# Kernel optimization log

Measured on AMD Instinct MI355X. Metric: run time of the kernel, lower is better.

## Reference

```python
import jax, jax.numpy as jnp
import numpy as np

N = 32768
LATENT = 2
HID = 100
STEPS = 100

swish = jax.nn.swish


def setup_inputs() -> dict:
    key = jax.random.key(0)
    ks = jax.random.split(key, 12)

    def w(k, shape):
        fan_in = shape[0]
        return (jax.random.normal(k, shape) / np.sqrt(fan_in)).astype(jnp.float32)

    return {
        "x": jax.random.normal(ks[0], (N, 3), dtype=jnp.float32),
        # encoder: 3 -> 100 -> 100 -> (mu: 2, log_t: 1)
        "We1": w(ks[1], (3, HID)), "be1": jnp.zeros((HID,), jnp.float32),
        "We2": w(ks[2], (HID, HID)), "be2": jnp.zeros((HID,), jnp.float32),
        "Wmu": w(ks[3], (HID, LATENT)), "bmu": jnp.zeros((LATENT,), jnp.float32),
        "Wlt": w(ks[4], (HID, 1)), "blt": jnp.zeros((1,), jnp.float32),
        # decoder: 2 -> 100 -> (mu: 3, log_sigma: 3)
        "Wd1": w(ks[5], (LATENT, HID)), "bd1": jnp.zeros((HID,), jnp.float32),
        "Wdmu": w(ks[6], (HID, 3)), "bdmu": jnp.zeros((3,), jnp.float32),
        "Wds": w(ks[7], (HID, 3)), "bds": jnp.zeros((3,), jnp.float32),
        # prior layer biases
        "b_muz": jnp.zeros((LATENT,), jnp.float32),
        "b_ltz": jnp.zeros((1,), jnp.float32),
        # standard-normal noise for the 100-step SDE (dW = sqrt(dt) * noise)
        "noise": jax.random.normal(ks[8], (STEPS, N, LATENT), dtype=jnp.float32),
    }


def reference(x, We1, be1, We2, be2, Wmu, bmu, Wlt, blt,
              Wd1, bd1, Wdmu, bdmu, Wds, bds, b_muz, b_ltz, noise):
    x = x.astype(jnp.float32)

    # ---- decoder heads on a single latent point z: (LATENT,) ----
    def dec_mu(z):
        return swish(z @ Wd1 + bd1) @ Wdmu + bdmu      # (3,)

    def dec_ls(z):
        return swish(z @ Wd1 + bd1) @ Wds + bds        # (3,)

    def G(z):  # pullback metric, (LATENT, LATENT)
        Jmu = jax.jacfwd(dec_mu)(z)   # (3, LATENT)
        Jsg = jax.jacfwd(dec_ls)(z)   # (3, LATENT)
        return Jmu.T @ Jmu + Jsg.T @ Jsg

    def step_one(z, dW):  # one Euler-Maruyama step for one point
        g = G(z)
        ginv = jnp.linalg.inv(g)
        Dg = jax.jacfwd(G)(z)         # (LATENT, LATENT, LATENT): dG[k,m]/dz_l
        Chris = 0.5 * (jnp.einsum('im,kml->ikl', ginv, Dg)
                       + jnp.einsum('im,lmk->ikl', ginv, Dg)
                       - jnp.einsum('im,klm->ikl', ginv, Dg))
        det = 0.5 * jnp.einsum('jk,ijk->i', ginv, Chris)
        stoch = ginv @ dW
        return (z + det + stoch).astype(jnp.float32)

    # ---- encoder ----
    h = swish(x @ We1 + be1)
    h = swish(h @ We2 + be2)
    mu_zx = h @ Wmu + bmu            # (N, LATENT)
    log_t_zx = h @ Wlt + blt         # (N, 1)

    # ---- Riemannian Brownian-motion sampling (Local) ----
    t = jnp.exp(2.0 * log_t_zx)[:, 0]        # (N,)
    dt = t / STEPS                            # (N,), constant over steps
    dW = jnp.sqrt(dt)[None, :, None] * noise  # (STEPS, N, LATENT)

    def scan_step(z, dW_t):
        return jax.vmap(step_one)(z, dW_t), None

    z, _ = jax.lax.scan(scan_step, mu_zx, dW)

    # ---- prior + decoder outputs ----
    mu_z = b_muz * jnp.ones_like(z)
    log_t_z = b_ltz * jnp.ones((z.shape[0], 1), z.dtype)
    hz = swish(z @ Wd1 + bd1)
    mu_xz = hz @ Wdmu + bdmu
    log_sigma_xz = hz @ Wds + bds

    return (z, mu_xz, log_sigma_xz, mu_zx, log_t_zx, mu_z, log_t_z)
```

## Files before the change

### kernel.cpp

```cpp
#include <hip/hip_runtime.h>

#define N_PTS 32768
#define HID   100
#define STEPS 100

#define OFF_Z     0
#define OFF_MUXZ  65536
#define OFF_LSXZ  163840
#define OFF_MUZX  262144
#define OFF_LTZX  327680
#define OFF_MUZ   360448
#define OFF_LTZ   425984

typedef float v2f __attribute__((ext_vector_type(2)));

#if __has_builtin(__builtin_elementwise_fma)
#define FMA2(a, b, c) __builtin_elementwise_fma((a), (b), (c))
#else
#define FMA2(a, b, c) ((a) * (b) + (c))
#endif

__device__ __forceinline__ v2f splat(float x) { v2f r; r.x = x; r.y = x; return r; }

__device__ __forceinline__ float qreduce(float v) {
  v += __int_as_float(__builtin_amdgcn_update_dpp(0, __float_as_int(v), 0xB1, 0xF, 0xF, true));
  v += __int_as_float(__builtin_amdgcn_update_dpp(0, __float_as_int(v), 0x4E, 0xF, 0xF, true));
  return v;
}
__device__ __forceinline__ v2f qreduce2(v2f v) {
  v2f r; r.x = qreduce(v.x); r.y = qreduce(v.y); return r;
}

__global__ __launch_bounds__(128, 1) void enc_kernel(
    const float* __restrict__ x,
    const float* __restrict__ We1, const float* __restrict__ be1,
    const float* __restrict__ We2, const float* __restrict__ be2,
    const float* __restrict__ Wmu, const float* __restrict__ bmu,
    const float* __restrict__ Wlt, const float* __restrict__ blt,
    const float* __restrict__ b_muz, const float* __restrict__ b_ltz,
    float* __restrict__ out)
{
  const int tid = threadIdx.x;
  const int w   = tid >> 6;
  const int pb  = tid & 63;
  const int p   = blockIdx.x * 64 + pb;
  const int ob  = __builtin_amdgcn_readfirstlane(w * 50);

  const float x0 = x[p*3+0], x1 = x[p*3+1], x2 = x[p*3+2];

  v2f acc2[25];
  #pragma unroll
  for (int i = 0; i < 25; ++i) { acc2[i].x = 0.f; acc2[i].y = 0.f; }

  for (int k = 0; k < HID; ++k) {
    float a   = fmaf(x0, We1[k], fmaf(x1, We1[HID+k], fmaf(x2, We1[2*HID+k], be1[k])));
    float sig = 1.f / (1.f + __expf(-a));
    float h1  = a * sig;
    const v2f hh = splat(h1);
    const v2f* row2 = (const v2f*)(We2 + k*HID + ob);
    #pragma unroll
    for (int oo = 0; oo < 25; ++oo) acc2[oo] = FMA2(hh, row2[oo], acc2[oo]);
  }

  float m0 = 0.f, m1 = 0.f, lt = 0.f;
  #pragma unroll
  for (int oo = 0; oo < 25; ++oo) {
    #pragma unroll
    for (int h = 0; h < 2; ++h) {
      const int o = ob + 2*oo + h;
      float a   = (h ? acc2[oo].y : acc2[oo].x) + be2[o];
      float sig = 1.f / (1.f + __expf(-a));
      float h2  = a * sig;
      m0 = fmaf(h2, Wmu[o*2+0], m0);
      m1 = fmaf(h2, Wmu[o*2+1], m1);
      lt = fmaf(h2, Wlt[o],     lt);
    }
  }

  __shared__ float red[2][64][3];
  red[w][pb][0] = m0; red[w][pb][1] = m1; red[w][pb][2] = lt;
  __syncthreads();
  if (w == 0) {
    m0 += red[1][pb][0] + bmu[0];
    m1 += red[1][pb][1] + bmu[1];
    lt += red[1][pb][2] + blt[0];
    out[OFF_MUZX + p*2+0] = m0;
    out[OFF_MUZX + p*2+1] = m1;
    out[OFF_LTZX + p]     = lt;
    out[OFF_MUZ  + p*2+0] = b_muz[0];
    out[OFF_MUZ  + p*2+1] = b_muz[1];
    out[OFF_LTZ  + p]     = b_ltz[0];
  }
}

__global__ __launch_bounds__(256, 2) void sde_kernel(
    const float* __restrict__ Wd1,  const float* __restrict__ bd1,
    const float* __restrict__ Wdmu, const float* __restrict__ bdmu,
    const float* __restrict__ Wds,  const float* __restrict__ bds,
    const float* __restrict__ noise,
    float* __restrict__ out)
{
  __shared__ __align__(16) float wrec[HID*12];
  const int tid = threadIdx.x;
  for (int idx = tid; idx < HID*12; idx += 256) {
    const int j = idx / 12, f = idx - j*12;
    const float w0 = Wd1[j], w1 = Wd1[HID + j];
    float v;
    switch (f) {
      case 0:  v = w0; break;
      case 1:  v = w1; break;
      case 2:  v = bd1[j]; break;
      case 3:  v = w0*w0; break;
      case 4:  v = w0*w1; break;
      case 5:  v = w1*w1; break;
      case 6:  v = Wdmu[j*3+0]; break;
      case 7:  v = Wds [j*3+0]; break;
      case 8:  v = Wdmu[j*3+1]; break;
      case 9:  v = Wds [j*3+1]; break;
      case 10: v = Wdmu[j*3+2]; break;
      default: v = Wds [j*3+2]; break;
    }
    wrec[idx] = v;
  }
  __syncthreads();

  const int l     = tid & 3;
  const int p     = blockIdx.x * 64 + (tid >> 2);
  const int jbase = l * 25;

  float z0 = out[OFF_MUZX + p*2+0];
  float z1 = out[OFF_MUZX + p*2+1];
  const float sdt = __expf(out[OFF_LTZX + p]) * 0.1f;

  const float2* __restrict__ noise2 = (const float2*)noise;

  for (int step = 0; step < STEPS; ++step) {
    const float2 nz = noise2[(size_t)step*N_PTS + p];

    v2f Jm2[3], Js2[3], Km01[3], Ks01[3], K2[3];
    #pragma unroll
    for (int o = 0; o < 3; ++o) {
      Jm2[o]=splat(0.f); Js2[o]=splat(0.f);
      Km01[o]=splat(0.f); Ks01[o]=splat(0.f); K2[o]=splat(0.f);
    }

    #pragma unroll 5
    for (int jj = 0; jj < 25; ++jj) {
      const float* r = &wrec[(jbase + jj)*12];
      const float4 wa = *(const float4*)(r);
      const float4 wb = *(const float4*)(r + 4);
      const float4 wc = *(const float4*)(r + 8);
      float a   = fmaf(z0, wa.x, fmaf(z1, wa.y, wa.z));
      float e   = __expf(-a);
      float sig = __builtin_amdgcn_rcpf(1.f + e);
      float t1  = 1.f - sig;
      float pp  = sig * t1;
      float u   = fmaf(a, pp, sig);
      float u2  = pp * fmaf(a, fmaf(-2.f, sig, 1.f), 2.f);
      v2f w01;   w01.x = wa.x;  w01.y = wa.y;
      v2f w0011; w0011.x = wa.w; w0011.y = wb.x;
      v2f c01   = splat(u)  * w01;
      v2f q0001 = splat(u2) * w0011;
      v2f q11s  = splat(u2 * wb.y);
      v2f ws[3];
      ws[0].x = wb.z; ws[0].y = wb.w;
      ws[1].x = wc.x; ws[1].y = wc.y;
      ws[2].x = wc.z; ws[2].y = wc.w;
      #pragma unroll
      for (int o = 0; o < 3; ++o) {
        const v2f mo = splat(ws[o].x);
        const v2f so = splat(ws[o].y);
        Jm2[o]  = FMA2(mo, c01,   Jm2[o]);
        Js2[o]  = FMA2(so, c01,   Js2[o]);
        Km01[o] = FMA2(mo, q0001, Km01[o]);
        Ks01[o] = FMA2(so, q0001, Ks01[o]);
        K2[o]   = FMA2(ws[o], q11s, K2[o]);
      }
    }

    float Jm[3][2], Js[3][2], Km[3][3], Ks[3][3];
    #pragma unroll
    for (int o = 0; o < 3; ++o) {
      v2f t;
      t = qreduce2(Jm2[o]);  Jm[o][0]=t.x; Jm[o][1]=t.y;
      t = qreduce2(Js2[o]);  Js[o][0]=t.x; Js[o][1]=t.y;
      t = qreduce2(Km01[o]); Km[o][0]=t.x; Km[o][1]=t.y;
      t = qreduce2(Ks01[o]); Ks[o][0]=t.x; Ks[o][1]=t.y;
      t = qreduce2(K2[o]);   Km[o][2]=t.x; Ks[o][2]=t.y;
    }

    float G00=0.f, G01=0.f, G11=0.f;
    #pragma unroll
    for (int o = 0; o < 3; ++o) {
      G00 += Jm[o][0]*Jm[o][0] + Js[o][0]*Js[o][0];
      G01 += Jm[o][0]*Jm[o][1] + Js[o][0]*Js[o][1];
      G11 += Jm[o][1]*Jm[o][1] + Js[o][1]*Js[o][1];
    }
    float D00=0.f, D01=0.f, D10=0.f, D11=0.f, D20=0.f, D21=0.f;
    #pragma unroll
    for (int o = 0; o < 3; ++o) {
      D00 += 2.f*(Km[o][0]*Jm[o][0] + Ks[o][0]*Js[o][0]);
      D01 += 2.f*(Km[o][1]*Jm[o][0] + Ks[o][1]*Js[o][0]);
      D10 += Km[o][0]*Jm[o][1] + Jm[o][0]*Km[o][1] + Ks[o][0]*Js[o][1] + Js[o][0]*Ks[o][1];
      D11 += Km[o][1]*Jm[o][1] + Jm[o][0]*Km[o][2] + Ks[o][1]*Js[o][1] + Js[o][0]*Ks[o][2];
      D20 += 2.f*(Km[o][1]*Jm[o][1] + Ks[o][1]*Js[o][1]);
      D21 += 2.f*(Km[o][2]*Jm[o][1] + Ks[o][2]*Js[o][1]);
    }
    const float det = fmaf(G00, G11, -G01*G01);
    const float id  = __builtin_amdgcn_rcpf(det);
    const float i00 = G11*id, i01 = -G01*id, i11 = G00*id;
    const float T000 = D00;
    const float T001 = 2.f*D10 - D01;
    const float T010 = D01;
    const float T011 = D20;
    const float T110 = 2.f*D11 - D20;
    const float T111 = D21;
    const float C00 = 0.5f*(i00*T000 + i01*T001);
    const float C01 = 0.5f*(i00*T010 + i01*T011);
    const float C02 = 0.5f*(i00*T110 + i01*T111);
    const float C10 = 0.5f*(i01*T000 + i11*T001);
    const float C11 = 0.5f*(i01*T010 + i11*T011);
    const float C12 = 0.5f*(i01*T110 + i11*T111);
    const float dr0 = 0.5f*(i00*C00 + 2.f*i01*C01 + i11*C02);
    const float dr1 = 0.5f*(i00*C10 + 2.f*i01*C11 + i11*C12);

    const float dw0 = sdt*nz.x, dw1 = sdt*nz.y;
    z0 += dr0 + i00*dw0 + i01*dw1;
    z1 += dr1 + i01*dw0 + i11*dw1;
  }

  v2f MS[3]; MS[0]=splat(0.f); MS[1]=splat(0.f); MS[2]=splat(0.f);
  #pragma unroll 5
  for (int jj = 0; jj < 25; ++jj) {
    const float* r = &wrec[(jbase + jj)*12];
    const float4 wa = *(const float4*)(r);
    const float4 wb = *(const float4*)(r + 4);
    const float4 wc = *(const float4*)(r + 8);
    float a   = fmaf(z0, wa.x, fmaf(z1, wa.y, wa.z));
    float sig = __builtin_amdgcn_rcpf(1.f + __expf(-a));
    float h   = a * sig;
    const v2f hh = splat(h);
    v2f ws0; ws0.x = wb.z; ws0.y = wb.w;
    v2f ws1; ws1.x = wc.x; ws1.y = wc.y;
    v2f ws2; ws2.x = wc.z; ws2.y = wc.w;
    MS[0] = FMA2(hh, ws0, MS[0]);
    MS[1] = FMA2(hh, ws1, MS[1]);
    MS[2] = FMA2(hh, ws2, MS[2]);
  }
  #pragma unroll
  for (int o = 0; o < 3; ++o) MS[o] = qreduce2(MS[o]);

  if (l == 0) {
    out[OFF_Z + p*2+0] = z0;
    out[OFF_Z + p*2+1] = z1;
    #pragma unroll
    for (int o = 0; o < 3; ++o) {
      out[OFF_MUXZ + p*3 + o] = MS[o].x + bdmu[o];
      out[OFF_LSXZ + p*3 + o] = MS[o].y + bds[o];
    }
  }
}

extern "C" void kernel_launch(void* const* d_in, const int* in_sizes, int n_in,
                              void* d_out, int out_size, void* d_ws, size_t ws_size,
                              hipStream_t stream) {
  (void)in_sizes; (void)n_in; (void)d_ws; (void)ws_size; (void)out_size;
  const float* x    = (const float*)d_in[0];
  const float* We1  = (const float*)d_in[1];
  const float* be1  = (const float*)d_in[2];
  const float* We2  = (const float*)d_in[3];
  const float* be2  = (const float*)d_in[4];
  const float* Wmu  = (const float*)d_in[5];
  const float* bmu  = (const float*)d_in[6];
  const float* Wlt  = (const float*)d_in[7];
  const float* blt  = (const float*)d_in[8];
  const float* Wd1  = (const float*)d_in[9];
  const float* bd1  = (const float*)d_in[10];
  const float* Wdmu = (const float*)d_in[11];
  const float* bdmu = (const float*)d_in[12];
  const float* Wds  = (const float*)d_in[13];
  const float* bds  = (const float*)d_in[14];
  const float* bmz  = (const float*)d_in[15];
  const float* blz  = (const float*)d_in[16];
  const float* noise= (const float*)d_in[17];
  float* out = (float*)d_out;

  enc_kernel<<<512, 128, 0, stream>>>(x, We1, be1, We2, be2, Wmu, bmu, Wlt, blt,
                                      bmz, blz, out);
  sde_kernel<<<512, 256, 0, stream>>>(Wd1, bd1, Wdmu, bdmu, Wds, bds, noise, out);
}
```

Before: 619.0 us.

## Pair hidden units in SDE packed math and split encoder across four waves

The SDE kernel's shared-memory weight table is reorganised so each record holds two hidden units interleaved. The inner loop then computes activations and Jacobian and Hessian accumulations for both units with packed v2f FMAs, and folds them with a horizontal add before the quad reduction. The aim is fewer scalar ops per hidden unit and more use of dual-issue packed FP32, at the cost of more accumulator registers and padding HID to 104. The encoder moves to 256 threads with four waves, each handling a quarter of the output columns, to raise parallelism and cut per-thread register pressure.

```diff
diff --git a/kernel.cpp b/kernel.cpp
--- a/kernel.cpp
+++ b/kernel.cpp
@@ -3,6 +3,8 @@
 #define N_PTS 32768
 #define HID   100
 #define STEPS 100
+#define NPAIR 52
+#define LPP   13
 
 #define OFF_Z     0
 #define OFF_MUXZ  65536
@@ -13,12 +15,15 @@
 #define OFF_LTZ   425984
 
 typedef float v2f __attribute__((ext_vector_type(2)));
+typedef float v4f __attribute__((ext_vector_type(4)));
 
 #if __has_builtin(__builtin_elementwise_fma)
 #define FMA2(a, b, c) __builtin_elementwise_fma((a), (b), (c))
 #else
 #define FMA2(a, b, c) ((a) * (b) + (c))
 #endif
+#define LOv(q) __builtin_shufflevector((q), (q), 0, 1)
+#define HIv(q) __builtin_shufflevector((q), (q), 2, 3)
 
 __device__ __forceinline__ v2f splat(float x) { v2f r; r.x = x; r.y = x; return r; }
 
@@ -27,11 +32,57 @@
   v += __int_as_float(__builtin_amdgcn_update_dpp(0, __float_as_int(v), 0x4E, 0xF, 0xF, true));
   return v;
 }
-__device__ __forceinline__ v2f qreduce2(v2f v) {
-  v2f r; r.x = qreduce(v.x); r.y = qreduce(v.y); return r;
-}
-
-__global__ __launch_bounds__(128, 1) void enc_kernel(
+__device__ __forceinline__ float hqreduce(v2f v) { return qreduce(v.x + v.y); }
+
+template<int NP>
+__device__ __forceinline__ void enc_chunk(
+    int ob, float x0, float x1, float x2,
+    const float* __restrict__ We1, const float* __restrict__ be1,
+    const float* __restrict__ We2, const float* __restrict__ be2,
+    const float* __restrict__ Wmu, const float* __restrict__ Wlt,
+    float& m0, float& m1, float& lt)
+{
+  v2f acc2[NP];
+  #pragma unroll
+  for (int i = 0; i < NP; ++i) acc2[i] = splat(0.f);
+
+  #pragma unroll 2
+  for (int k = 0; k < HID; k += 2) {
+    const v2f w0 = *(const v2f*)(We1 + k);
+    const v2f w1 = *(const v2f*)(We1 + HID + k);
+    const v2f w2 = *(const v2f*)(We1 + 2*HID + k);
+    const v2f bb = *(const v2f*)(be1 + k);
+    v2f aP = FMA2(splat(x0), w0, FMA2(splat(x1), w1, FMA2(splat(x2), w2, bb)));
+    const float e0 = __expf(-aP.x), e1 = __expf(-aP.y);
+    const float s0 = 1.f / (1.f + e0), s1 = 1.f / (1.f + e1);
+    const v2f hh0 = splat(aP.x * s0);
+    const v2f hh1 = splat(aP.y * s1);
+    const v2f* r0 = (const v2f*)(We2 + k*HID + ob);
+    const v2f* r1 = (const v2f*)(We2 + (k+1)*HID + ob);
+    #pragma unroll
+    for (int oo = 0; oo < NP; ++oo) {
+      v2f tacc = FMA2(hh0, r0[oo], acc2[oo]);
+      acc2[oo] = FMA2(hh1, r1[oo], tacc);
+    }
+  }
+
+  m0 = 0.f; m1 = 0.f; lt = 0.f;
+  #pragma unroll
+  for (int oo = 0; oo < NP; ++oo) {
+    #pragma unroll
+    for (int h = 0; h < 2; ++h) {
+      const int o = ob + 2*oo + h;
+      float a   = (h ? acc2[oo].y : acc2[oo].x) + be2[o];
+      float sig = 1.f / (1.f + __expf(-a));
+      float h2  = a * sig;
+      m0 = fmaf(h2, Wmu[o*2+0], m0);
+      m1 = fmaf(h2, Wmu[o*2+1], m1);
+      lt = fmaf(h2, Wlt[o],     lt);
+    }
+  }
+}
+
+__global__ __launch_bounds__(256, 2) void enc_kernel(
     const float* __restrict__ x,
     const float* __restrict__ We1, const float* __restrict__ be1,
     const float* __restrict__ We2, const float* __restrict__ be2,
@@ -44,46 +95,20 @@
   const int w   = tid >> 6;
   const int pb  = tid & 63;
   const int p   = blockIdx.x * 64 + pb;
-  const int ob  = __builtin_amdgcn_readfirstlane(w * 50);
 
   const float x0 = x[p*3+0], x1 = x[p*3+1], x2 = x[p*3+2];
 
-  v2f acc2[25];
-  #pragma unroll
-  for (int i = 0; i < 25; ++i) { acc2[i].x = 0.f; acc2[i].y = 0.f; }
-
-  for (int k = 0; k < HID; ++k) {
-    float a   = fmaf(x0, We1[k], fmaf(x1, We1[HID+k], fmaf(x2, We1[2*HID+k], be1[k])));
-    float sig = 1.f / (1.f + __expf(-a));
-    float h1  = a * sig;
-    const v2f hh = splat(h1);
-    const v2f* row2 = (const v2f*)(We2 + k*HID + ob);
-    #pragma unroll
-    for (int oo = 0; oo < 25; ++oo) acc2[oo] = FMA2(hh, row2[oo], acc2[oo]);
-  }
-
-  float m0 = 0.f, m1 = 0.f, lt = 0.f;
-  #pragma unroll
-  for (int oo = 0; oo < 25; ++oo) {
-    #pragma unroll
-    for (int h = 0; h < 2; ++h) {
-      const int o = ob + 2*oo + h;
-      float a   = (h ? acc2[oo].y : acc2[oo].x) + be2[o];
-      float sig = 1.f / (1.f + __expf(-a));
-      float h2  = a * sig;
-      m0 = fmaf(h2, Wmu[o*2+0], m0);
-      m1 = fmaf(h2, Wmu[o*2+1], m1);
-      lt = fmaf(h2, Wlt[o],     lt);
-    }
-  }
-
-  __shared__ float red[2][64][3];
+  float m0, m1, lt;
+  if (w < 2) enc_chunk<13>(w * 26,            x0, x1, x2, We1, be1, We2, be2, Wmu, Wlt, m0, m1, lt);
+  else       enc_chunk<12>(52 + (w - 2) * 24, x0, x1, x2, We1, be1, We2, be2, Wmu, Wlt, m0, m1, lt);
+
+  __shared__ float red[4][64][3];
   red[w][pb][0] = m0; red[w][pb][1] = m1; red[w][pb][2] = lt;
   __syncthreads();
   if (w == 0) {
-    m0 += red[1][pb][0] + bmu[0];
-    m1 += red[1][pb][1] + bmu[1];
-    lt += red[1][pb][2] + blt[0];
+    m0 += red[1][pb][0] + red[2][pb][0] + red[3][pb][0] + bmu[0];
+    m1 += red[1][pb][1] + red[2][pb][1] + red[3][pb][1] + bmu[1];
+    lt += red[1][pb][2] + red[2][pb][2] + red[3][pb][2] + blt[0];
     out[OFF_MUZX + p*2+0] = m0;
     out[OFF_MUZX + p*2+1] = m1;
     out[OFF_LTZX + p]     = lt;
@@ -100,25 +125,29 @@
     const float* __restrict__ noise,
     float* __restrict__ out)
 {
-  __shared__ __align__(16) float wrec[HID*12];
+  __shared__ __align__(16) float wrec[NPAIR * 24];
   const int tid = threadIdx.x;
-  for (int idx = tid; idx < HID*12; idx += 256) {
-    const int j = idx / 12, f = idx - j*12;
-    const float w0 = Wd1[j], w1 = Wd1[HID + j];
-    float v;
-    switch (f) {
-      case 0:  v = w0; break;
-      case 1:  v = w1; break;
-      case 2:  v = bd1[j]; break;
-      case 3:  v = w0*w0; break;
-      case 4:  v = w0*w1; break;
-      case 5:  v = w1*w1; break;
-      case 6:  v = Wdmu[j*3+0]; break;
-      case 7:  v = Wds [j*3+0]; break;
-      case 8:  v = Wdmu[j*3+1]; break;
-      case 9:  v = Wds [j*3+1]; break;
-      case 10: v = Wdmu[j*3+2]; break;
-      default: v = Wds [j*3+2]; break;
+  for (int idx = tid; idx < NPAIR * 24; idx += 256) {
+    const int pr = idx / 24, f = idx - pr * 24;
+    const int j  = pr * 2 + (f & 1);
+    const int g  = f >> 1;
+    float v = 0.f;
+    if (j < HID) {
+      const float w0 = Wd1[j], w1 = Wd1[HID + j];
+      switch (g) {
+        case 0:  v = w0; break;
+        case 1:  v = w1; break;
+        case 2:  v = bd1[j]; break;
+        case 3:  v = w1 * w1; break;
+        case 4:  v = w0 * w0; break;
+        case 5:  v = w0 * w1; break;
+        case 6:  v = Wdmu[j*3+0]; break;
+        case 7:  v = Wds [j*3+0]; break;
+        case 8:  v = Wdmu[j*3+1]; break;
+        case 9:  v = Wds [j*3+1]; break;
+        case 10: v = Wdmu[j*3+2]; break;
+        default: v = Wds [j*3+2]; break;
+      }
     }
     wrec[idx] = v;
   }
@@ -126,7 +155,8 @@
 
   const int l     = tid & 3;
   const int p     = blockIdx.x * 64 + (tid >> 2);
-  const int jbase = l * 25;
+  const int pbase = l * LPP;
+  const v4f* __restrict__ Rq = (const v4f*)wrec;
 
   float z0 = out[OFF_MUZX + p*2+0];
   float z1 = out[OFF_MUZX + p*2+1];
@@ -135,76 +165,82 @@
   const float2* __restrict__ noise2 = (const float2*)noise;
 
   for (int step = 0; step < STEPS; ++step) {
-    const float2 nz = noise2[(size_t)step*N_PTS + p];
-
-    v2f Jm2[3], Js2[3], Km01[3], Ks01[3], K2[3];
-    #pragma unroll
-    for (int o = 0; o < 3; ++o) {
-      Jm2[o]=splat(0.f); Js2[o]=splat(0.f);
-      Km01[o]=splat(0.f); Ks01[o]=splat(0.f); K2[o]=splat(0.f);
-    }
-
-    #pragma unroll 5
-    for (int jj = 0; jj < 25; ++jj) {
-      const float* r = &wrec[(jbase + jj)*12];
-      const float4 wa = *(const float4*)(r);
-      const float4 wb = *(const float4*)(r + 4);
-      const float4 wc = *(const float4*)(r + 8);
-      float a   = fmaf(z0, wa.x, fmaf(z1, wa.y, wa.z));
-      float e   = __expf(-a);
-      float sig = __builtin_amdgcn_rcpf(1.f + e);
-      float t1  = 1.f - sig;
-      float pp  = sig * t1;
-      float u   = fmaf(a, pp, sig);
-      float u2  = pp * fmaf(a, fmaf(-2.f, sig, 1.f), 2.f);
-      v2f w01;   w01.x = wa.x;  w01.y = wa.y;
-      v2f w0011; w0011.x = wa.w; w0011.y = wb.x;
-      v2f c01   = splat(u)  * w01;
-      v2f q0001 = splat(u2) * w0011;
-      v2f q11s  = splat(u2 * wb.y);
-      v2f ws[3];
-      ws[0].x = wb.z; ws[0].y = wb.w;
-      ws[1].x = wc.x; ws[1].y = wc.y;
-      ws[2].x = wc.z; ws[2].y = wc.w;
+    const float2 nz = noise2[(size_t)step * N_PTS + p];
+
+    v2f Jm[3][2], Js[3][2], Km[3][3], Ks[3][3];
+    #pragma unroll
+    for (int o = 0; o < 3; ++o) {
+      Jm[o][0]=splat(0.f); Jm[o][1]=splat(0.f);
+      Js[o][0]=splat(0.f); Js[o][1]=splat(0.f);
+      Km[o][0]=splat(0.f); Km[o][1]=splat(0.f); Km[o][2]=splat(0.f);
+      Ks[o][0]=splat(0.f); Ks[o][1]=splat(0.f); Ks[o][2]=splat(0.f);
+    }
+    const v2f z0P = splat(z0), z1P = splat(z1);
+
+    #pragma unroll
+    for (int t = 0; t < LPP; ++t) {
+      const v4f* R = Rq + (pbase + t) * 6;
+      const v4f A  = R[0];
+      const v4f B  = R[1];
+      const v4f Cq = R[2];
+      const v4f M0 = R[3], M1 = R[4], M2 = R[5];
+      const v2f W0P  = LOv(A),  W1P  = HIv(A);
+      const v2f bP   = LOv(B),  W11P = HIv(B);
+      const v2f W00P = LOv(Cq), W01P = HIv(Cq);
+
+      v2f aP = FMA2(z0P, W0P, FMA2(z1P, W1P, bP));
+      v2f eP;   eP.x   = __expf(-aP.x);               eP.y   = __expf(-aP.y);
+      v2f dP = splat(1.f) + eP;
+      v2f sigP; sigP.x = __builtin_amdgcn_rcpf(dP.x); sigP.y = __builtin_amdgcn_rcpf(dP.y);
+      const v2f t1P = splat(1.f) - sigP;
+      const v2f ppP = sigP * t1P;
+      const v2f uP  = FMA2(aP, ppP, sigP);
+      const v2f u2P = ppP * FMA2(aP, FMA2(splat(-2.f), sigP, splat(1.f)), splat(2.f));
+      const v2f c0  = uP  * W0P,  c1  = uP  * W1P;
+      const v2f q00 = u2P * W00P, q01 = u2P * W01P, q11 = u2P * W11P;
+
+      const v2f mP[3] = {LOv(M0), LOv(M1), LOv(M2)};
+      const v2f sP[3] = {HIv(M0), HIv(M1), HIv(M2)};
       #pragma unroll
       for (int o = 0; o < 3; ++o) {
-        const v2f mo = splat(ws[o].x);
-        const v2f so = splat(ws[o].y);
-        Jm2[o]  = FMA2(mo, c01,   Jm2[o]);
-        Js2[o]  = FMA2(so, c01,   Js2[o]);
-        Km01[o] = FMA2(mo, q0001, Km01[o]);
-        Ks01[o] = FMA2(so, q0001, Ks01[o]);
-        K2[o]   = FMA2(ws[o], q11s, K2[o]);
+        Jm[o][0] = FMA2(c0,  mP[o], Jm[o][0]);
+        Jm[o][1] = FMA2(c1,  mP[o], Jm[o][1]);
+        Js[o][0] = FMA2(c0,  sP[o], Js[o][0]);
+        Js[o][1] = FMA2(c1,  sP[o], Js[o][1]);
+        Km[o][0] = FMA2(q00, mP[o], Km[o][0]);
+        Km[o][1] = FMA2(q01, mP[o], Km[o][1]);
+        Km[o][2] = FMA2(q11, mP[o], Km[o][2]);
+        Ks[o][0] = FMA2(q00, sP[o], Ks[o][0]);
+        Ks[o][1] = FMA2(q01, sP[o], Ks[o][1]);
+        Ks[o][2] = FMA2(q11, sP[o], Ks[o][2]);
       }
     }
 
-    float Jm[3][2], Js[3][2], Km[3][3], Ks[3][3];
-    #pragma unroll
-    for (int o = 0; o < 3; ++o) {
-      v2f t;
-      t = qreduce2(Jm2[o]);  Jm[o][0]=t.x; Jm[o][1]=t.y;
-      t = qreduce2(Js2[o]);  Js[o][0]=t.x; Js[o][1]=t.y;
-      t = qreduce2(Km01[o]); Km[o][0]=t.x; Km[o][1]=t.y;
-      t = qreduce2(Ks01[o]); Ks[o][0]=t.x; Ks[o][1]=t.y;
-      t = qreduce2(K2[o]);   Km[o][2]=t.x; Ks[o][2]=t.y;
+    float JmS[3][2], JsS[3][2], KmS[3][3], KsS[3][3];
+    #pragma unroll
+    for (int o = 0; o < 3; ++o) {
+      JmS[o][0]=hqreduce(Jm[o][0]); JmS[o][1]=hqreduce(Jm[o][1]);
+      JsS[o][0]=hqreduce(Js[o][0]); JsS[o][1]=hqreduce(Js[o][1]);
+      KmS[o][0]=hqreduce(Km[o][0]); KmS[o][1]=hqreduce(Km[o][1]); KmS[o][2]=hqreduce(Km[o][2]);
+      KsS[o][0]=hqreduce(Ks[o][0]); KsS[o][1]=hqreduce(Ks[o][1]); KsS[o][2]=hqreduce(Ks[o][2]);
     }
 
     float G00=0.f, G01=0.f, G11=0.f;
     #pragma unroll
     for (int o = 0; o < 3; ++o) {
-      G00 += Jm[o][0]*Jm[o][0] + Js[o][0]*Js[o][0];
-      G01 += Jm[o][0]*Jm[o][1] + Js[o][0]*Js[o][1];
-      G11 += Jm[o][1]*Jm[o][1] + Js[o][1]*Js[o][1];
+      G00 += JmS[o][0]*JmS[o][0] + JsS[o][0]*JsS[o][0];
+      G01 += JmS[o][0]*JmS[o][1] + JsS[o][0]*JsS[o][1];
+      G11 += JmS[o][1]*JmS[o][1] + JsS[o][1]*JsS[o][1];
     }
     float D00=0.f, D01=0.f, D10=0.f, D11=0.f, D20=0.f, D21=0.f;
     #pragma unroll
     for (int o = 0; o < 3; ++o) {
-      D00 += 2.f*(Km[o][0]*Jm[o][0] + Ks[o][0]*Js[o][0]);
-      D01 += 2.f*(Km[o][1]*Jm[o][0] + Ks[o][1]*Js[o][0]);
-      D10 += Km[o][0]*Jm[o][1] + Jm[o][0]*Km[o][1] + Ks[o][0]*Js[o][1] + Js[o][0]*Ks[o][1];
-      D11 += Km[o][1]*Jm[o][1] + Jm[o][0]*Km[o][2] + Ks[o][1]*Js[o][1] + Js[o][0]*Ks[o][2];
-      D20 += 2.f*(Km[o][1]*Jm[o][1] + Ks[o][1]*Js[o][1]);
-      D21 += 2.f*(Km[o][2]*Jm[o][1] + Ks[o][2]*Js[o][1]);
+      D00 += 2.f*(KmS[o][0]*JmS[o][0] + KsS[o][0]*JsS[o][0]);
+      D01 += 2.f*(KmS[o][1]*JmS[o][0] + KsS[o][1]*JsS[o][0]);
+      D10 += KmS[o][0]*JmS[o][1] + JmS[o][0]*KmS[o][1] + KsS[o][0]*JsS[o][1] + JsS[o][0]*KsS[o][1];
+      D11 += KmS[o][1]*JmS[o][1] + JmS[o][0]*KmS[o][2] + KsS[o][1]*JsS[o][1] + JsS[o][0]*KsS[o][2];
+      D20 += 2.f*(KmS[o][1]*JmS[o][1] + KsS[o][1]*JsS[o][1]);
+      D21 += 2.f*(KmS[o][2]*JmS[o][1] + KsS[o][2]*JsS[o][1]);
     }
     const float det = fmaf(G00, G11, -G01*G01);
     const float id  = __builtin_amdgcn_rcpf(det);
@@ -229,34 +265,36 @@
     z1 += dr1 + i01*dw0 + i11*dw1;
   }
 
-  v2f MS[3]; MS[0]=splat(0.f); MS[1]=splat(0.f); MS[2]=splat(0.f);
-  #pragma unroll 5
-  for (int jj = 0; jj < 25; ++jj) {
-    const float* r = &wrec[(jbase + jj)*12];
-    const float4 wa = *(const float4*)(r);
-    const float4 wb = *(const float4*)(r + 4);
-    const float4 wc = *(const float4*)(r + 8);
-    float a   = fmaf(z0, wa.x, fmaf(z1, wa.y, wa.z));
-    float sig = __builtin_amdgcn_rcpf(1.f + __expf(-a));
-    float h   = a * sig;
-    const v2f hh = splat(h);
-    v2f ws0; ws0.x = wb.z; ws0.y = wb.w;
-    v2f ws1; ws1.x = wc.x; ws1.y = wc.y;
-    v2f ws2; ws2.x = wc.z; ws2.y = wc.w;
-    MS[0] = FMA2(hh, ws0, MS[0]);
-    MS[1] = FMA2(hh, ws1, MS[1]);
-    MS[2] = FMA2(hh, ws2, MS[2]);
-  }
-  #pragma unroll
-  for (int o = 0; o < 3; ++o) MS[o] = qreduce2(MS[o]);
+  v2f MSm[3], MSs[3];
+  #pragma unroll
+  for (int o = 0; o < 3; ++o) { MSm[o] = splat(0.f); MSs[o] = splat(0.f); }
+  const v2f zf0 = splat(z0), zf1 = splat(z1);
+  #pragma unroll
+  for (int t = 0; t < LPP; ++t) {
+    const v4f* R = Rq + (pbase + t) * 6;
+    const v4f A  = R[0];
+    const v4f B  = R[1];
+    const v4f M0 = R[3], M1 = R[4], M2 = R[5];
+    v2f aP = FMA2(zf0, LOv(A), FMA2(zf1, HIv(A), LOv(B)));
+    v2f eP;   eP.x   = __expf(-aP.x);               eP.y   = __expf(-aP.y);
+    v2f dP = splat(1.f) + eP;
+    v2f sigP; sigP.x = __builtin_amdgcn_rcpf(dP.x); sigP.y = __builtin_amdgcn_rcpf(dP.y);
+    const v2f hP = aP * sigP;
+    MSm[0] = FMA2(hP, LOv(M0), MSm[0]);  MSs[0] = FMA2(hP, HIv(M0), MSs[0]);
+    MSm[1] = FMA2(hP, LOv(M1), MSm[1]);  MSs[1] = FMA2(hP, HIv(M1), MSs[1]);
+    MSm[2] = FMA2(hP, LOv(M2), MSm[2]);  MSs[2] = FMA2(hP, HIv(M2), MSs[2]);
+  }
+  float mu[3], ls[3];
+  #pragma unroll
+  for (int o = 0; o < 3; ++o) { mu[o] = hqreduce(MSm[o]); ls[o] = hqreduce(MSs[o]); }
 
   if (l == 0) {
     out[OFF_Z + p*2+0] = z0;
     out[OFF_Z + p*2+1] = z1;
     #pragma unroll
     for (int o = 0; o < 3; ++o) {
-      out[OFF_MUXZ + p*3 + o] = MS[o].x + bdmu[o];
-      out[OFF_LSXZ + p*3 + o] = MS[o].y + bds[o];
+      out[OFF_MUXZ + p*3 + o] = mu[o] + bdmu[o];
+      out[OFF_LSXZ + p*3 + o] = ls[o] + bds[o];
     }
   }
 }
@@ -285,7 +323,7 @@
   const float* noise= (const float*)d_in[17];
   float* out = (float*)d_out;
 
-  enc_kernel<<<512, 128, 0, stream>>>(x, We1, be1, We2, be2, Wmu, bmu, Wlt, blt,
+  enc_kernel<<<512, 256, 0, stream>>>(x, We1, be1, We2, be2, Wmu, bmu, Wlt, blt,
                                       bmz, blz, out);
   sde_kernel<<<512, 256, 0, stream>>>(Wd1, bd1, Wdmu, bdmu, Wds, bds, noise, out);
 }
```

Result: slower. 1.431 ms (+131.1%).
